# Performance work log

Hardware: AMD Instinct MI355X
Metric: run time of the kernel (lower is better)

Reference implementation:

```python
import jax, jax.numpy as jnp
import numpy as np

N_ROUTES = 7      # len(ROUTES): 3 unimodal + 3 bimodal + 1 trimodal routes
PC_DIM = 512      # primary capsule pose dim
MC_DIM = 128      # output (decision) capsule pose dim
K = 25            # num_classes (phenotypes)
NUM_ROUTING = 3   # routing iterations
B = 4096


def _layer_norm(x, gamma, beta, eps=1e-5):
    mu = jnp.mean(x, axis=-1, keepdims=True)
    var = jnp.var(x, axis=-1, keepdims=True)
    return (x - mu) * jax.lax.rsqrt(var + eps) * gamma + beta


def setup_inputs() -> dict:
    key = jax.random.key(0)
    ks = jax.random.split(key, 4)
    w_std = float(np.sqrt(K / (PC_DIM * N_ROUTES)))  # CapsuleFC weight init scale
    return {
        "prim_pose": jax.random.normal(ks[0], (B, N_ROUTES, PC_DIM), dtype=jnp.float32),
        "prim_act": jax.random.uniform(ks[1], (B, N_ROUTES), dtype=jnp.float32),
        "w": w_std * jax.random.normal(ks[2], (N_ROUTES, PC_DIM, K, MC_DIM), dtype=jnp.float32),
        "ln_gamma": jnp.ones((MC_DIM,), dtype=jnp.float32),
        "ln_beta": jnp.zeros((MC_DIM,), dtype=jnp.float32),
        "embedding": 0.02 * jax.random.normal(ks[3], (K, MC_DIM), dtype=jnp.float32),
        "bias": jnp.zeros((K,), dtype=jnp.float32),
    }


def reference(prim_pose, prim_act, w, ln_gamma, ln_beta, embedding, bias):
    # prim_pose: [B, N, D_in]; prim_act: [B, N]
    act = prim_act[..., None]                      # [B, N, 1]
    scale = 1.0 / np.sqrt(MC_DIM)
    # Votes are constant across routing iterations; hoist out of the loop.
    vote = jnp.einsum('bnd,ndmv->bnmv', prim_pose, w)  # [B, N, K, Dv]
    next_pose = None
    routing_coef = None
    for it in range(NUM_ROUTING):
        if next_pose is None:
            # iteration 0: uniform routing coefficients (softmax of zeros over out capsules)
            routing_coef = jnp.full((prim_pose.shape[0], N_ROUTES, K), 1.0 / K,
                                    dtype=prim_pose.dtype)
        else:
            # inverted dot-product attention: agreement between votes and current decision pose
            agree = jnp.einsum('bnmv,bmv->bnm', vote, next_pose) * scale
            routing_coef = jax.nn.softmax(agree, axis=-1)
        c = routing_coef * act                     # weight routing by primary activations
        next_pose = _layer_norm(jnp.einsum('bnm,bnmv->bmv', c, vote), ln_gamma, ln_beta)
        # act_type='ONES' -> decision activations are all ones (no effect on routing)
    logits = jnp.einsum('bmd,md->bm', next_pose, embedding) + bias  # [B, K]
    return logits, prim_act, routing_coef
```

## Files before the change

kernel.cpp:

```cpp
#include <hip/hip_runtime.h>
#include <hip/hip_bf16.h>
#include <math.h>

#define N_ROUTES 7
#define PC_DIM   512
#define MC_DIM   128
#define KCLS     25
#define BATCH    4096

#define ROW_IN   (N_ROUTES * PC_DIM)
#define JDIM     (KCLS * MC_DIM)
#define VOTE_B   (N_ROUTES * JDIM)

typedef __attribute__((ext_vector_type(8))) _Float16 half8;
typedef __attribute__((ext_vector_type(4))) float f32x4;

__device__ inline ushort f2h(float f) {
    _Float16 h = (_Float16)f;
    return __builtin_bit_cast(ushort, h);
}

__device__ inline float2 h2f2(uint u) {
    union { uint x; _Float16 h[2]; } c; c.x = u;
    return make_float2((float)c.h[0], (float)c.h[1]);
}

__device__ inline void load_lds16(const void* g, void* l) {
    __builtin_amdgcn_global_load_lds(
        (const __attribute__((address_space(1))) void*)g,
        (__attribute__((address_space(3))) void*)l, 16, 0, 0);
}

__global__ __launch_bounds__(256) void conv_pose(const float* __restrict__ p,
                                                 ushort* __restrict__ pb, int n8) {
    int i = blockIdx.x * 256 + threadIdx.x;
    if (i >= n8) return;
    const float4* s = (const float4*)p + (size_t)i * 2;
    float4 a = s[0], b = s[1];
    ushort t[8];
    t[0]=f2h(a.x); t[1]=f2h(a.y); t[2]=f2h(a.z); t[3]=f2h(a.w);
    t[4]=f2h(b.x); t[5]=f2h(b.y); t[6]=f2h(b.z); t[7]=f2h(b.w);
    *(uint4*)(pb + (size_t)i * 8) = *(uint4*)t;
}

__global__ __launch_bounds__(256) void conv_w(const float* __restrict__ w,
                                              ushort* __restrict__ wt) {
    __shared__ float t[32][33];
    const int j0 = blockIdx.x * 32, d0 = blockIdx.y * 32, r = blockIdx.z;
    const int c = threadIdx.x & 31, rr = threadIdx.x >> 5;
    const float* wp = w + (size_t)r * PC_DIM * JDIM;
#pragma unroll
    for (int i = 0; i < 4; i++)
        t[rr + i * 8][c] = wp[(size_t)(d0 + rr + i * 8) * JDIM + j0 + c];
    __syncthreads();
    ushort* op = wt + (size_t)r * JDIM * PC_DIM;
#pragma unroll
    for (int i = 0; i < 4; i++)
        op[(size_t)(j0 + rr + i * 8) * PC_DIM + d0 + c] = f2h(t[c][rr + i * 8]);
}

#define GBM 128
#define GBN 128
#define GBK 64

__global__ __launch_bounds__(256) void vote_gemm_mfma(
        const ushort* __restrict__ poseb,
        const ushort* __restrict__ wt,
        ushort* __restrict__ vote,
        int rows) {
    const int id = blockIdx.x;
    const int rowTile = id / (N_ROUTES * 25);
    const int rem = id - rowTile * (N_ROUTES * 25);
    const int route = rem / 25;
    const int jTile = rem - route * 25;
    const int b0 = rowTile * GBM;
    const int j0 = jTile * GBN;

    __shared__ __align__(16) char smem[32768];
    ushort* As = (ushort*)smem;
    ushort* Bs = As + GBM * GBK;

    const int tid = threadIdx.x;
    const int l = tid & 63, w = tid >> 6;
    const int wm = w >> 1, wn = w & 1;

    f32x4 acc[4][4] = {};

    const ushort* Aptr = poseb + (size_t)route * PC_DIM;
    const ushort* Bptr = wt + (size_t)route * JDIM * PC_DIM;

    const int q4 = l >> 4;
    const int swz = l & 7;

    for (int k0 = 0; k0 < PC_DIM; k0 += GBK) {
        int f = tid;
#pragma unroll
        for (int i = 0; i < 4; i++, f += 256) {
            const int row = f >> 3;
            const int c = f & 7;
            const int qg = c ^ (row & 7);
            int ga = b0 + row; if (ga >= rows) ga = rows - 1;
            load_lds16(Aptr + (size_t)ga * ROW_IN + k0 + qg * 8, As + (size_t)f * 8);
            load_lds16(Bptr + (size_t)(j0 + row) * PC_DIM + k0 + qg * 8, Bs + (size_t)f * 8);
        }
        __syncthreads();

#pragma unroll
        for (int s = 0; s < 2; s++) {
            half8 af[4], bfg[4];
#pragma unroll
            for (int t = 0; t < 4; t++) {
                const int rowA = wm * 64 + t * 16 + (l & 15);
                const int rowB = wn * 64 + t * 16 + (l & 15);
                const int c = (s * 4 + q4) ^ swz;
                af[t]  = *(const half8*)(As + (size_t)(rowA * 8 + c) * 8);
                bfg[t] = *(const half8*)(Bs + (size_t)(rowB * 8 + c) * 8);
            }
#pragma unroll
            for (int mt = 0; mt < 4; mt++)
#pragma unroll
                for (int nt = 0; nt < 4; nt++)
                    acc[mt][nt] = __builtin_amdgcn_mfma_f32_16x16x32_f16(
                        af[mt], bfg[nt], acc[mt][nt], 0, 0, 0);
        }
        __syncthreads();
    }

    float* ep = (float*)smem + w * 16 * 68;
    const int erow = l >> 2;
    const int ec0  = (l & 3) * 16;
#pragma unroll
    for (int mt = 0; mt < 4; mt++) {
#pragma unroll
        for (int nt = 0; nt < 4; nt++)
#pragma unroll
            for (int i = 0; i < 4; i++)
                ep[((l >> 4) * 4 + i) * 68 + nt * 16 + (l & 15)] = acc[mt][nt][i];
        __syncthreads();
        const int grow = b0 + wm * 64 + mt * 16 + erow;
        if (grow < rows) {
            ushort t16[16];
#pragma unroll
            for (int t8 = 0; t8 < 4; t8++) {
                float4 v = *(float4*)&ep[erow * 68 + ec0 + t8 * 4];
                t16[t8*4+0]=f2h(v.x); t16[t8*4+1]=f2h(v.y);
                t16[t8*4+2]=f2h(v.z); t16[t8*4+3]=f2h(v.w);
            }
            ushort* dst = vote + (size_t)grow * VOTE_B + route * JDIM + j0 + wn * 64 + ec0;
            ((uint4*)dst)[0] = ((uint4*)t16)[0];
            ((uint4*)dst)[1] = ((uint4*)t16)[1];
        }
        __syncthreads();
    }
}

__global__ __launch_bounds__(512) void routing_kernel(
        const ushort* __restrict__ vote16,
        const float* __restrict__ act,
        const float* __restrict__ gamma,
        const float* __restrict__ beta,
        const float* __restrict__ emb,
        const float* __restrict__ bias,
        float* __restrict__ out_logits,
        float* __restrict__ out_act,
        float* __restrict__ out_coef) {
    const int b = blockIdx.x;
    __shared__ float coef_s[N_ROUTES * KCLS];
    __shared__ float act_s[8];

    const int tid = threadIdx.x, l = tid & 63, wv = tid >> 6;
    const int sub = l & 15, mg = l >> 4;
    const int m = wv + 8 * mg;
    const bool mv = (m < KCLS);
    const int mc = mv ? m : 24;

    if (tid < N_ROUTES) {
        float a = act[(size_t)b * N_ROUTES + tid];
        act_s[tid] = a;
        out_act[(size_t)b * N_ROUTES + tid] = a;
    }

    uint4 v[N_ROUTES];
    const uint4* vb = (const uint4*)(vote16 + (size_t)b * VOTE_B);
#pragma unroll
    for (int n = 0; n < N_ROUTES; n++)
        v[n] = vb[n * 400 + mc * 16 + sub];

    float g[8], be[8];
    *(float4*)(g)      = *(const float4*)(gamma + 8 * sub);
    *(float4*)(g + 4)  = *(const float4*)(gamma + 8 * sub + 4);
    *(float4*)(be)     = *(const float4*)(beta  + 8 * sub);
    *(float4*)(be + 4) = *(const float4*)(beta  + 8 * sub + 4);
    __syncthreads();

    const float scale = 0.088388347648318447f;
    float pose[8];

    auto update = [&](bool first) {
        float r[8];
#pragma unroll
        for (int j = 0; j < 8; j++) r[j] = 0.f;
#pragma unroll
        for (int n = 0; n < N_ROUTES; n++) {
            float c = first ? (act_s[n] * 0.04f) : (coef_s[n * KCLS + mc] * act_s[n]);
            float2 f0 = h2f2(v[n].x), f1 = h2f2(v[n].y), f2 = h2f2(v[n].z), f3 = h2f2(v[n].w);
            r[0] += c * f0.x; r[1] += c * f0.y; r[2] += c * f1.x; r[3] += c * f1.y;
            r[4] += c * f2.x; r[5] += c * f2.y; r[6] += c * f3.x; r[7] += c * f3.y;
        }
        float S = 0.f, Q = 0.f;
#pragma unroll
        for (int j = 0; j < 8; j++) { S += r[j]; Q += r[j] * r[j]; }
#pragma unroll
        for (int o = 8; o; o >>= 1) {
            S += __shfl_xor(S, o);
            Q += __shfl_xor(Q, o);
        }
        float mean = S * 0.0078125f;
        float var  = Q * 0.0078125f - mean * mean;
        float rs   = rsqrtf(var + 1e-5f);
#pragma unroll
        for (int j = 0; j < 8; j++) pose[j] = (r[j] - mean) * rs * g[j] + be[j];
        __syncthreads();
    };

    update(true);

    for (int it = 1; it < 3; it++) {
        float d[N_ROUTES];
#pragma unroll
        for (int n = 0; n < N_ROUTES; n++) {
            float2 f0 = h2f2(v[n].x), f1 = h2f2(v[n].y), f2 = h2f2(v[n].z), f3 = h2f2(v[n].w);
            d[n] = f0.x * pose[0] + f0.y * pose[1] + f1.x * pose[2] + f1.y * pose[3]
                 + f2.x * pose[4] + f2.y * pose[5] + f3.x * pose[6] + f3.y * pose[7];
        }
#pragma unroll
        for (int o = 8; o; o >>= 1)
#pragma unroll
            for (int n = 0; n < N_ROUTES; n++) d[n] += __shfl_xor(d[n], o);
        if (sub == 0 && mv) {
#pragma unroll
            for (int n = 0; n < N_ROUTES; n++) coef_s[n * KCLS + m] = d[n] * scale;
        }
        __syncthreads();
        if (tid < N_ROUTES) {
            float mx = -1e30f;
            for (int mm = 0; mm < KCLS; mm++) mx = fmaxf(mx, coef_s[tid * KCLS + mm]);
            float s = 0.f;
            float e[KCLS];
            for (int mm = 0; mm < KCLS; mm++) { e[mm] = expf(coef_s[tid * KCLS + mm] - mx); s += e[mm]; }
            float inv = 1.0f / s;
            for (int mm = 0; mm < KCLS; mm++) coef_s[tid * KCLS + mm] = e[mm] * inv;
        }
        __syncthreads();
        update(false);
    }

    float e[8];
    *(float4*)(e)     = *(const float4*)(emb + mc * MC_DIM + 8 * sub);
    *(float4*)(e + 4) = *(const float4*)(emb + mc * MC_DIM + 8 * sub + 4);
    float dd = 0.f;
#pragma unroll
    for (int j = 0; j < 8; j++) dd += pose[j] * e[j];
#pragma unroll
    for (int o = 8; o; o >>= 1) dd += __shfl_xor(dd, o);
    if (sub == 0 && mv) out_logits[(size_t)b * KCLS + m] = dd + bias[m];

    if (tid < N_ROUTES * KCLS)
        out_coef[(size_t)b * (N_ROUTES * KCLS) + tid] = coef_s[tid];
}

extern "C" void kernel_launch(void* const* d_in, const int* in_sizes, int n_in,
                              void* d_out, int out_size, void* d_ws, size_t ws_size,
                              hipStream_t stream) {
    const float* pose  = (const float*)d_in[0];
    const float* act   = (const float*)d_in[1];
    const float* w     = (const float*)d_in[2];
    const float* gamma = (const float*)d_in[3];
    const float* beta  = (const float*)d_in[4];
    const float* emb   = (const float*)d_in[5];
    const float* bias  = (const float*)d_in[6];

    float* out        = (float*)d_out;
    float* out_logits = out;
    float* out_act    = out + BATCH * KCLS;
    float* out_coef   = out + BATCH * KCLS + BATCH * N_ROUTES;

    const size_t wt_bytes    = (size_t)N_ROUTES * JDIM * PC_DIM * 2;
    const size_t poseb_bytes = (size_t)BATCH * ROW_IN * 2;
    ushort* wt    = (ushort*)d_ws;
    ushort* poseb = (ushort*)((char*)d_ws + wt_bytes);
    ushort* voteh = (ushort*)((char*)d_ws + wt_bytes + poseb_bytes);

    size_t rem = ws_size > wt_bytes + poseb_bytes ? ws_size - wt_bytes - poseb_bytes : 0;
    size_t cap = rem / ((size_t)VOTE_B * 2);
    int chunk;
    if (cap >= (size_t)BATCH)  chunk = BATCH;
    else if (cap >= 128)       chunk = (int)(cap & ~(size_t)127);
    else                       chunk = (int)(cap > 0 ? cap : 1);

    conv_w<<<dim3(JDIM / 32, PC_DIM / 32, N_ROUTES), 256, 0, stream>>>(w, wt);
    const int n8 = BATCH * ROW_IN / 8;
    conv_pose<<<(n8 + 255) / 256, 256, 0, stream>>>(pose, poseb, n8);

    for (int b0 = 0; b0 < BATCH; b0 += chunk) {
        int rows = BATCH - b0 < chunk ? BATCH - b0 : chunk;
        int nRowTiles = (rows + GBM - 1) / GBM;
        vote_gemm_mfma<<<nRowTiles * N_ROUTES * 25, 256, 0, stream>>>(
            poseb + (size_t)b0 * ROW_IN, wt, voteh, rows);
        routing_kernel<<<rows, 512, 0, stream>>>(
            voteh,
            act + (size_t)b0 * N_ROUTES,
            gamma, beta, emb, bias,
            out_logits + (size_t)b0 * KCLS,
            out_act    + (size_t)b0 * N_ROUTES,
            out_coef   + (size_t)b0 * N_ROUTES * KCLS);
    }
}
```

Baseline: 395.4 us.

## Remap GEMM block order for locality, parallelize routing softmax across lanes

The vote GEMM block index mapping is changed to group blocks (8-way interleave across route/rowTile, presumably for XCD/L2 locality) when the grid size is 5600, with a generic fallback ordering otherwise. In the routing kernel, invalid capsule lanes skip the vote loads, and the per-route softmax moves from 7 serial threads to 7 groups of 32 lanes using shuffle reductions. This aims to cut L2 misses in the GEMM and shorten the serial softmax section between barriers.

```diff
diff --git a/kernel.cpp b/kernel.cpp
--- a/kernel.cpp
+++ b/kernel.cpp
@@ -68,11 +68,22 @@
         const ushort* __restrict__ wt,
         ushort* __restrict__ vote,
         int rows) {
-    const int id = blockIdx.x;
-    const int rowTile = id / (N_ROUTES * 25);
-    const int rem = id - rowTile * (N_ROUTES * 25);
-    const int route = rem / 25;
-    const int jTile = rem - route * 25;
+    int route, rowTile, jTile;
+    if (gridDim.x == 5600) {
+        const int x = blockIdx.x & 7;
+        const int g = blockIdx.x >> 3;
+        const int q = g / 25;
+        jTile = g - q * 25;
+        const int p = x * 28 + q;
+        route = p >> 5;
+        rowTile = p & 31;
+    } else {
+        const int nrt = gridDim.x / (N_ROUTES * 25);
+        route = blockIdx.x / (nrt * 25);
+        const int r2 = blockIdx.x - route * nrt * 25;
+        rowTile = r2 / 25;
+        jTile = r2 - rowTile * 25;
+    }
     const int b0 = rowTile * GBM;
     const int j0 = jTile * GBN;
 
@@ -172,7 +183,6 @@
     const int sub = l & 15, mg = l >> 4;
     const int m = wv + 8 * mg;
     const bool mv = (m < KCLS);
-    const int mc = mv ? m : 24;
 
     if (tid < N_ROUTES) {
         float a = act[(size_t)b * N_ROUTES + tid];
@@ -180,11 +190,14 @@
         out_act[(size_t)b * N_ROUTES + tid] = a;
     }
 
-    uint4 v[N_ROUTES];
-    const uint4* vb = (const uint4*)(vote16 + (size_t)b * VOTE_B);
-#pragma unroll
-    for (int n = 0; n < N_ROUTES; n++)
-        v[n] = vb[n * 400 + mc * 16 + sub];
+    uint4 v[N_ROUTES] = {};
+    if (mv) {
+        const uint4* vb = (const uint4*)(vote16 + (size_t)b * VOTE_B);
+#pragma unroll
+        for (int n = 0; n < N_ROUTES; n++)
+            v[n] = vb[n * 400 + m * 16 + sub];
+    }
+    const int mc = mv ? m : 24;
 
     float g[8], be[8];
     *(float4*)(g)      = *(const float4*)(gamma + 8 * sub);
@@ -225,6 +238,8 @@
 
     update(true);
 
+    const int sgrp = tid >> 5, slane = tid & 31;
+
     for (int it = 1; it < 3; it++) {
         float d[N_ROUTES];
 #pragma unroll
@@ -242,14 +257,16 @@
             for (int n = 0; n < N_ROUTES; n++) coef_s[n * KCLS + m] = d[n] * scale;
         }
         __syncthreads();
-        if (tid < N_ROUTES) {
-            float mx = -1e30f;
-            for (int mm = 0; mm < KCLS; mm++) mx = fmaxf(mx, coef_s[tid * KCLS + mm]);
-            float s = 0.f;
-            float e[KCLS];
-            for (int mm = 0; mm < KCLS; mm++) { e[mm] = expf(coef_s[tid * KCLS + mm] - mx); s += e[mm]; }
-            float inv = 1.0f / s;
-            for (int mm = 0; mm < KCLS; mm++) coef_s[tid * KCLS + mm] = e[mm] * inv;
+        if (sgrp < N_ROUTES) {
+            float c = (slane < KCLS) ? coef_s[sgrp * KCLS + slane] : -1e30f;
+            float mx = c;
+#pragma unroll
+            for (int o = 16; o; o >>= 1) mx = fmaxf(mx, __shfl_xor(mx, o, 32));
+            float e = (slane < KCLS) ? expf(c - mx) : 0.f;
+            float s = e;
+#pragma unroll
+            for (int o = 16; o; o >>= 1) s += __shfl_xor(s, o, 32);
+            if (slane < KCLS) coef_s[sgrp * KCLS + slane] = e / s;
         }
         __syncthreads();
         update(false);
```

New measurement: 376.1 us. -4.9%, faster.
